# Optimization experiments

Measured on AMD Instinct MI355X. Metric: run time of the kernel, lower is better.

The kernel has to match this reference:

```python
import jax, jax.numpy as jnp
import numpy as np

N, E, G = 50000, 400000, 2048
H, C = 4, 64            # heads, hidden per head
IN, ED, TASKS = 29, 6, 12
HC = H * C


def setup_inputs() -> dict:
    key = jax.random.key(0)
    ks = jax.random.split(key, 20)
    s = 0.1
    f32 = jnp.float32
    inp = {
        'x': jax.random.normal(ks[0], (N, IN), f32),
        'edge_index': jax.random.randint(ks[1], (2, E), 0, N),
        'edge_attr': jax.random.normal(ks[2], (E, ED), f32),
        'batch': jnp.sort(jax.random.randint(ks[3], (N,), 0, G)),
        # layer 1 (in=29 -> H*C=256)
        'W1': jax.random.normal(ks[4], (IN, HC), f32) * s,
        'as1': jax.random.normal(ks[5], (1, H, C), f32) * s,
        'ad1': jax.random.normal(ks[6], (1, H, C), f32) * s,
        'We1': jax.random.normal(ks[7], (ED, HC), f32) * s,
        'ae1': jax.random.normal(ks[8], (1, H, C), f32) * s,
        'b1': jnp.zeros((HC,), f32),
        # layer 2 (in=256 -> 256)
        'W2': jax.random.normal(ks[9], (HC, HC), f32) * s,
        'as2': jax.random.normal(ks[10], (1, H, C), f32) * s,
        'ad2': jax.random.normal(ks[11], (1, H, C), f32) * s,
        'We2': jax.random.normal(ks[12], (ED, HC), f32) * s,
        'ae2': jax.random.normal(ks[13], (1, H, C), f32) * s,
        'b2': jnp.zeros((HC,), f32),
        # readout linear (256 -> 12)
        'Wl': jax.random.normal(ks[14], (HC, TASKS), f32) * s,
        'bl': jnp.zeros((TASKS,), f32),
    }
    return inp


def _gat_conv(x, src, dst, eattr, W, a_src, a_dst, We, a_e, b):
    """PyG GATConv, concat=True, leaky_relu slope 0.2, self-loops already appended."""
    h = (x @ W).reshape(N, H, C)                      # [N,H,C]
    al_s = jnp.sum(h * a_src, axis=-1)                # [N,H]
    al_d = jnp.sum(h * a_dst, axis=-1)                # [N,H]
    he = (eattr @ We).reshape(-1, H, C)               # [Etot,H,C]
    al_e = jnp.sum(he * a_e, axis=-1)                 # [Etot,H]
    alpha = al_s[src] + al_d[dst] + al_e              # [Etot,H]
    alpha = jax.nn.leaky_relu(alpha, negative_slope=0.2)
    # segment softmax over incoming edges of each dst node
    amax = jax.ops.segment_max(alpha, dst, num_segments=N)
    ex = jnp.exp(alpha - amax[dst])
    denom = jax.ops.segment_sum(ex, dst, num_segments=N)
    alpha = ex / (denom[dst] + 1e-16)
    msg = h[src] * alpha[:, :, None]                  # [Etot,H,C]
    out = jax.ops.segment_sum(msg, dst, num_segments=N)
    return out.reshape(N, HC) + b


def reference(x, edge_index, edge_attr, batch,
              W1, as1, ad1, We1, ae1, b1,
              W2, as2, ad2, We2, ae2, b2, Wl, bl):
    # add self-loops with edge_attr fill = mean over existing edges (PyG default)
    loop = jnp.arange(N)
    src = jnp.concatenate([edge_index[0], loop])
    dst = jnp.concatenate([edge_index[1], loop])
    mean_e = jnp.mean(edge_attr, axis=0, keepdims=True)
    eattr = jnp.concatenate([edge_attr, jnp.broadcast_to(mean_e, (N, ED))], axis=0)

    h = _gat_conv(x, src, dst, eattr, W1, as1, ad1, We1, ae1, b1)
    h = jax.nn.relu(h)
    h = _gat_conv(h, src, dst, eattr, W2, as2, ad2, We2, ae2, b2)
    h = jax.nn.relu(h)

    # global mean pool over graphs
    sums = jax.ops.segment_sum(h, batch, num_segments=G)      # [G,HC]
    cnt = jax.ops.segment_sum(jnp.ones((N,), h.dtype), batch, num_segments=G)
    pooled = sums / jnp.maximum(cnt, 1.0)[:, None]
    return pooled @ Wl + bl
```

## Files before the change

kernel.cpp:

```cpp
#include <hip/hip_runtime.h>
#include <math.h>

static constexpr int NN = 50000;
static constexpr int EE = 400000;
static constexpr int GG = 2048;
static constexpr int TASKS = 12;

typedef __attribute__((ext_vector_type(8))) short short8;
typedef __attribute__((ext_vector_type(4))) float floatx4;

__device__ __forceinline__ unsigned short f2bf(float f) {
  unsigned u = __float_as_uint(f);
  u = u + 0x7fffu + ((u >> 16) & 1u);
  return (unsigned short)(u >> 16);
}
__device__ __forceinline__ float bflo(unsigned u) { return __uint_as_float(u << 16); }
__device__ __forceinline__ float bfhi(unsigned u) { return __uint_as_float(u & 0xffff0000u); }

static constexpr int NBDEG = (EE + 255) / 256;
static constexpr int NBMEAN = 256;
static constexpr int NBX = (NN * 4 + 255) / 256;
static constexpr int NW1 = 32;
static constexpr int NW2 = 256;
__global__ void k_pre(const int* __restrict__ dst, const float* __restrict__ ea,
                      const float* __restrict__ x, const float* __restrict__ W1,
                      const float* __restrict__ W2, int* __restrict__ deg,
                      float* __restrict__ msum, unsigned short* __restrict__ xb,
                      unsigned short* __restrict__ w1t, unsigned short* __restrict__ w2t) {
  const int b = blockIdx.x;
  const int t = threadIdx.x;
  if (b < NBDEG) {
    int e = b * 256 + t;
    if (e < EE) atomicAdd(&deg[dst[e]], 1);
  } else if (b < NBDEG + NBMEAN) {
    float s[6] = {0, 0, 0, 0, 0, 0};
    for (int e = (b - NBDEG) * 256 + t; e < EE; e += NBMEAN * 256) {
#pragma unroll
      for (int d = 0; d < 6; d++) s[d] += ea[(size_t)e * 6 + d];
    }
    __shared__ float ls[6];
    if (t < 6) ls[t] = 0.f;
    __syncthreads();
#pragma unroll
    for (int d = 0; d < 6; d++) atomicAdd(&ls[d], s[d]);
    __syncthreads();
    if (t < 6) atomicAdd(&msum[t], ls[t]);
  } else if (b < NBDEG + NBMEAN + NBX) {
    int i = (b - NBDEG - NBMEAN) * 256 + t;
    if (i < NN * 4) {
      int n = i >> 2, seg = i & 3;
      unsigned short v[8];
#pragma unroll
      for (int j = 0; j < 8; j++) {
        int k = seg * 8 + j;
        v[j] = (k < 29) ? f2bf(x[(size_t)n * 29 + k]) : (unsigned short)0;
      }
      *(short8*)(xb + (size_t)n * 32 + seg * 8) = *(short8*)v;
    }
  } else if (b < NBDEG + NBMEAN + NBX + NW1) {
    int i = (b - NBDEG - NBMEAN - NBX) * 256 + t;
    int row = i >> 5, k = i & 31;
    unsigned short v = (k < 29) ? f2bf(W1[(size_t)k * 256 + row]) : (unsigned short)0;
    w1t[((row >> 4) * 4 + (k >> 3)) * 128 + (row & 15) * 8 + (k & 7)] = v;
  } else {
    int i = (b - NBDEG - NBMEAN - NBX - NW1) * 256 + t;
    int row = i >> 8, k = i & 255;
    w2t[((row >> 4) * 32 + (k >> 3)) * 128 + (row & 15) * 8 + (k & 7)] = f2bf(W2[(size_t)k * 256 + row]);
  }
}

__global__ void k_scan1(const int* __restrict__ deg, int* __restrict__ rowptr, int* __restrict__ bsums) {
  __shared__ int sh[256];
  int i = blockIdx.x * 256 + threadIdx.x;
  int v = (i < NN) ? deg[i] : 0;
  sh[threadIdx.x] = v;
  __syncthreads();
  for (int off = 1; off < 256; off <<= 1) {
    int t = (threadIdx.x >= off) ? sh[threadIdx.x - off] : 0;
    __syncthreads();
    sh[threadIdx.x] += t;
    __syncthreads();
  }
  if (i < NN) rowptr[i] = sh[threadIdx.x] - v;
  if (threadIdx.x == 255) bsums[blockIdx.x] = sh[255];
}

__global__ void k_scan23(int* __restrict__ rowptr, const int* __restrict__ bsums, int nb) {
  __shared__ int sh[256];
  const int t = threadIdx.x;
  sh[t] = (t < nb) ? bsums[t] : 0;
  __syncthreads();
  for (int off = 1; off < 256; off <<= 1) {
    int tv = (t >= off) ? sh[t - off] : 0;
    __syncthreads();
    sh[t] += tv;
    __syncthreads();
  }
  const int add = (blockIdx.x == 0) ? 0 : sh[blockIdx.x - 1];
  int i = blockIdx.x * 256 + t;
  if (i < NN) rowptr[i] += add;
  if (i == 0) rowptr[NN] = EE;
}

template <int KP>
__device__ __forceinline__ void gemm_body(
    int bx, const unsigned short* __restrict__ A, const unsigned short* __restrict__ Bt,
    const float* __restrict__ a_s, const float* __restrict__ a_d,
    unsigned short* __restrict__ Y, float* __restrict__ als, float* __restrict__ ald, int M) {
  __shared__ __align__(16) unsigned short Ash[64 * KP];
  const int tid = threadIdx.x;
  const int lane = tid & 63;
  const int w = tid >> 6;
  const int l15 = lane & 15;
  const int quad = lane >> 4;
  const int row0 = bx * 64;

  constexpr int STEPS = (64 * KP * 2) / (256 * 16);
  {
    const char* Ab = (const char*)(A + (size_t)row0 * KP);
    uint4 stg[STEPS];
#pragma unroll
    for (int s = 0; s < STEPS; s++) stg[s] = *(const uint4*)(Ab + s * 4096 + tid * 16);
#pragma unroll
    for (int s = 0; s < STEPS; s++) {
      int o = s * 4096 + tid * 16;
      int row = o / (KP * 2);
      *(uint4*)((char*)Ash + (o ^ ((row & 7) << 4))) = stg[s];
    }
  }

  floatx4 acc[4][4];
#pragma unroll
  for (int i = 0; i < 4; i++)
#pragma unroll
    for (int j = 0; j < 4; j++) acc[i][j] = {0.f, 0.f, 0.f, 0.f};

  const unsigned short* pb[4];
#pragma unroll
  for (int j = 0; j < 4; j++)
    pb[j] = Bt + (size_t)((w * 4 + j) * (KP / 8) + quad) * 128 + l15 * 8;

  constexpr int NPH = KP / 32;
  short8 bfr[2][4];
#pragma unroll
  for (int j = 0; j < 4; j++) bfr[0][j] = *(const short8*)pb[j];

  __syncthreads();

#pragma unroll
  for (int ph = 0; ph < NPH; ph++) {
    const int cur = ph & 1, nxt = cur ^ 1;
    if (ph + 1 < NPH) {
#pragma unroll
      for (int j = 0; j < 4; j++) {
        pb[j] += 512;
        bfr[nxt][j] = *(const short8*)pb[j];
      }
    }
    short8 af[4];
#pragma unroll
    for (int i = 0; i < 4; i++) {
      int lin = (i * 16 + l15) * (KP * 2) + ph * 64 + quad * 16;
      af[i] = *(const short8*)((const char*)Ash + (lin ^ (((lin / (KP * 2)) & 7) << 4)));
    }
#pragma unroll
    for (int i = 0; i < 4; i++)
#pragma unroll
      for (int j = 0; j < 4; j++)
        acc[i][j] = __builtin_amdgcn_mfma_f32_16x16x32_bf16(af[i], bfr[cur][j], acc[i][j], 0, 0, 0);
  }
  float asc[4], adc[4];
#pragma unroll
  for (int j = 0; j < 4; j++) {
    asc[j] = a_s[w * 64 + j * 16 + l15];
    adc[j] = a_d[w * 64 + j * 16 + l15];
  }
#pragma unroll
  for (int i = 0; i < 4; i++) {
#pragma unroll
    for (int r = 0; r < 4; r++) {
      const int row = row0 + i * 16 + quad * 4 + r;
      unsigned ub[4];
      float hv[4];
#pragma unroll
      for (int j = 0; j < 4; j++) {
        ub[j] = f2bf(acc[i][j][r]);
        hv[j] = __uint_as_float(ub[j] << 16);
      }
      if (row < M) {
#pragma unroll
        for (int j = 0; j < 4; j++) Y[(size_t)row * 256 + w * 64 + j * 16 + l15] = (unsigned short)ub[j];
      }
      float ps = hv[0] * asc[0] + hv[1] * asc[1] + hv[2] * asc[2] + hv[3] * asc[3];
      float pd = hv[0] * adc[0] + hv[1] * adc[1] + hv[2] * adc[2] + hv[3] * adc[3];
#pragma unroll
      for (int off = 1; off < 16; off <<= 1) {
        ps += __shfl_xor(ps, off, 64);
        pd += __shfl_xor(pd, off, 64);
      }
      if (l15 == 0 && row < M) {
        als[row * 4 + w] = ps;
        ald[row * 4 + w] = pd;
      }
    }
  }
}

static constexpr int GB = (NN + 63) / 64;

__global__ __launch_bounds__(256, 2) void k_scatgemm1(
    const int* __restrict__ ei, const int* __restrict__ rowptr, int* __restrict__ cursor,
    int* __restrict__ csrc, int* __restrict__ eslot, const float* __restrict__ We1,
    const float* __restrict__ ae1, const float* __restrict__ We2, const float* __restrict__ ae2,
    const float* __restrict__ msum, float* __restrict__ p1, float* __restrict__ p2,
    const unsigned short* __restrict__ xb, const unsigned short* __restrict__ w1t,
    const float* __restrict__ as1, const float* __restrict__ ad1,
    unsigned short* __restrict__ hb, float* __restrict__ als, float* __restrict__ ald) {
  const int b = blockIdx.x;
  const int t = threadIdx.x;
  if (b < NBDEG) {
    int e = b * 256 + t;
    if (e >= EE) return;
    int s = ei[e];
    int d = ei[EE + e];
    int p = atomicAdd(&cursor[d], 1);
    int slot = rowptr[d] + p;
    csrc[slot] = s;
    eslot[e] = slot;
  } else if (b < NBDEG + 2) {
    const int layer = b - NBDEG;
    const float* We = layer ? We2 : We1;
    const float* ae = layer ? ae2 : ae1;
    float* params = layer ? p2 : p1;
    __shared__ float vsh[24];
    if (t < 24) {
      int d = t >> 2, h = t & 3;
      float s = 0.f;
      for (int c = 0; c < 64; c++) s += We[d * 256 + h * 64 + c] * ae[h * 64 + c];
      vsh[t] = s;
      params[t] = s;
    }
    __syncthreads();
    if (t < 4) {
      float s = 0.f;
      const float invE = 1.0f / (float)EE;
#pragma unroll
      for (int d = 0; d < 6; d++) s += (msum[d] * invE) * vsh[d * 4 + t];
      params[24 + t] = s;
    }
  } else {
    gemm_body<32>(b - NBDEG - 2, xb, w1t, as1, ad1, hb, als, ald, NN);
  }
}

__global__ __launch_bounds__(256, 2) void k_gemm2(
    const unsigned short* __restrict__ A, const unsigned short* __restrict__ Bt,
    const float* __restrict__ a_s, const float* __restrict__ a_d,
    unsigned short* __restrict__ Y, float* __restrict__ als, float* __restrict__ ald) {
  gemm_body<256>(blockIdx.x, A, Bt, a_s, a_d, Y, als, ald, NN);
}

__device__ __forceinline__ float leaky02(float x) { return x > 0.f ? x : 0.2f * x; }

__global__ void k_edge(const int* __restrict__ ei, const float* __restrict__ ea,
                       const float* __restrict__ als, const float* __restrict__ ald,
                       const int* __restrict__ eslot, const float* __restrict__ params,
                       float* __restrict__ exa) {
  int e = blockIdx.x * blockDim.x + threadIdx.x;
  if (e >= EE) return;
  int src = ei[e], dst = ei[EE + e];
  float4 s4 = *(const float4*)(als + (size_t)src * 4);
  float4 d4 = *(const float4*)(ald + (size_t)dst * 4);
  float ed[6];
#pragma unroll
  for (int d = 0; d < 6; d++) ed[d] = ea[(size_t)e * 6 + d];
  float sl[4] = {s4.x + d4.x, s4.y + d4.y, s4.z + d4.z, s4.w + d4.w};
  float out[4];
#pragma unroll
  for (int h = 0; h < 4; h++) {
    float x = sl[h];
#pragma unroll
    for (int d = 0; d < 6; d++) x += ed[d] * params[d * 4 + h];
    out[h] = __expf(leaky02(x));
  }
  *(float4*)(exa + (size_t)eslot[e] * 4) = make_float4(out[0], out[1], out[2], out[3]);
}

__global__ __launch_bounds__(256) void k_agg(
    const unsigned short* __restrict__ hinb, const float* __restrict__ als,
    const float* __restrict__ ald, const int* __restrict__ rowptr, const int* __restrict__ csrc,
    const float* __restrict__ exa, const float* __restrict__ params, const float* __restrict__ bias,
    unsigned short* __restrict__ houtb) {
  const int lane = threadIdx.x & 63;
  const int n = blockIdx.x * 4 + (threadIdx.x >> 6);
  if (n >= NN) return;
  const int half = lane >> 5;
  const int sl = lane & 31;
  const int head = sl >> 3;

  float acc[8];
  float ssum;
  {
    float slg = leaky02(als[n * 4 + head] + ald[n * 4 + head] + params[24 + head]);
    float exs = __expf(slg);
    float wgt = (half == 0) ? exs : 0.f;
    ssum = wgt;
    uint4 uv = *(const uint4*)(hinb + (size_t)n * 256 + sl * 8);
    acc[0] = bflo(uv.x) * wgt;
    acc[1] = bfhi(uv.x) * wgt;
    acc[2] = bflo(uv.y) * wgt;
    acc[3] = bfhi(uv.y) * wgt;
    acc[4] = bflo(uv.z) * wgt;
    acc[5] = bfhi(uv.z) * wgt;
    acc[6] = bflo(uv.w) * wgt;
    acc[7] = bfhi(uv.w) * wgt;
  }
  const int end = rowptr[n + 1];
  int s = rowptr[n] + half;
  while (s < end) {
    int sid[4];
    float ex[4];
#pragma unroll
    for (int k = 0; k < 4; k++) {
      const int q = s + 2 * k;
      const bool v = q < end;
      const int idx = v ? q : end - 1;
      sid[k] = csrc[idx];
      ex[k] = v ? exa[(size_t)idx * 4 + head] : 0.f;
    }
    uint4 r[4];
#pragma unroll
    for (int k = 0; k < 4; k++) {
      r[k] = make_uint4(0u, 0u, 0u, 0u);
      if (s + 2 * k < end) r[k] = *(const uint4*)(hinb + (size_t)sid[k] * 256 + sl * 8);
    }
#pragma unroll
    for (int k = 0; k < 4; k++) {
      acc[0] += bflo(r[k].x) * ex[k];
      acc[1] += bfhi(r[k].x) * ex[k];
      acc[2] += bflo(r[k].y) * ex[k];
      acc[3] += bfhi(r[k].y) * ex[k];
      acc[4] += bflo(r[k].z) * ex[k];
      acc[5] += bfhi(r[k].z) * ex[k];
      acc[6] += bflo(r[k].w) * ex[k];
      acc[7] += bfhi(r[k].w) * ex[k];
      ssum += ex[k];
    }
    s += 8;
  }
#pragma unroll
  for (int j = 0; j < 8; j++) acc[j] += __shfl_xor(acc[j], 32, 64);
  ssum += __shfl_xor(ssum, 32, 64);
  if (half == 0) {
    const float inv = 1.f / (ssum + 1e-16f);
    float4 b0 = *(const float4*)(bias + sl * 8);
    float4 b1 = *(const float4*)(bias + sl * 8 + 4);
    const float bb[8] = {b0.x, b0.y, b0.z, b0.w, b1.x, b1.y, b1.z, b1.w};
    uint p[4];
#pragma unroll
    for (int j = 0; j < 4; j++) {
      float e0 = fmaxf(acc[2 * j] * inv + bb[2 * j], 0.f);
      float e1 = fmaxf(acc[2 * j + 1] * inv + bb[2 * j + 1], 0.f);
      p[j] = (uint)f2bf(e0) | ((uint)f2bf(e1) << 16);
    }
    *(uint4*)(houtb + (size_t)n * 256 + sl * 8) = make_uint4(p[0], p[1], p[2], p[3]);
  }
}

__global__ __launch_bounds__(256) void k_pool(const unsigned short* __restrict__ hb,
                                              const int* __restrict__ batch,
                                              const float* __restrict__ Wl,
                                              const float* __restrict__ bl,
                                              float* __restrict__ out) {
  int g = blockIdx.x;
  int t = threadIdx.x;
  int lo = 0, hi = NN;
  while (lo < hi) {
    int mid = (lo + hi) >> 1;
    if (batch[mid] < g) lo = mid + 1; else hi = mid;
  }
  int start = lo;
  hi = NN;
  while (lo < hi) {
    int mid = (lo + hi) >> 1;
    if (batch[mid] < g + 1) lo = mid + 1; else hi = mid;
  }
  int end = lo;
  const int mid2 = start + ((end - start) >> 1);
  __shared__ float sp[256], sq[256];
  {
    const int c = t & 127;
    const int hseg = t >> 7;
    const int a = hseg ? mid2 : start;
    const int b = hseg ? end : mid2;
    float s0 = 0.f, s1 = 0.f;
    for (int n2 = a; n2 < b; n2++) {
      uint u = ((const uint*)(hb + (size_t)n2 * 256))[c];
      s0 += bflo(u);
      s1 += bfhi(u);
    }
    float* dst = hseg ? sq : sp;
    dst[2 * c] = s0;
    dst[2 * c + 1] = s1;
  }
  __syncthreads();
  if (t < TASKS) {
    float invc = 1.f / fmaxf((float)(end - start), 1.f);
    float o = bl[t];
    for (int c = 0; c < 256; c++) o += (sp[c] + sq[c]) * invc * Wl[c * 12 + t];
    out[(size_t)g * 12 + t] = o;
  }
}

extern "C" void kernel_launch(void* const* d_in, const int* in_sizes, int n_in,
                              void* d_out, int out_size, void* d_ws, size_t ws_size,
                              hipStream_t stream) {
  const float* x = (const float*)d_in[0];
  const int* ei = (const int*)d_in[1];
  const float* ea = (const float*)d_in[2];
  const int* batch = (const int*)d_in[3];
  const float* W1 = (const float*)d_in[4];
  const float* as1 = (const float*)d_in[5];
  const float* ad1 = (const float*)d_in[6];
  const float* We1 = (const float*)d_in[7];
  const float* ae1 = (const float*)d_in[8];
  const float* b1 = (const float*)d_in[9];
  const float* W2 = (const float*)d_in[10];
  const float* as2 = (const float*)d_in[11];
  const float* ad2 = (const float*)d_in[12];
  const float* We2 = (const float*)d_in[13];
  const float* ae2 = (const float*)d_in[14];
  const float* b2 = (const float*)d_in[15];
  const float* Wl = (const float*)d_in[16];
  const float* bl = (const float*)d_in[17];
  float* out = (float*)d_out;

  char* ws = (char*)d_ws;
  size_t off = 0;
  auto take = [&](size_t bytes) -> char* {
    char* p = ws + off;
    off = (off + bytes + 255) & ~(size_t)255;
    return p;
  };
  float* msum = (float*)take(8 * 4);
  int* deg = (int*)take((size_t)NN * 4);
  int* cursor = (int*)take((size_t)NN * 4);
  size_t zero_end = off;
  int* rowptr = (int*)take((size_t)(NN + 1) * 4);
  int* bsums = (int*)take(256 * 4);
  int* csrc = (int*)take((size_t)EE * 4);
  int* eslot = (int*)take((size_t)EE * 4);
  float* exa = (float*)take((size_t)EE * 4 * 4);
  float* p1 = (float*)take(32 * 4);
  float* p2 = (float*)take(32 * 4);
  float* als = (float*)take((size_t)NN * 4 * 4);
  float* ald = (float*)take((size_t)NN * 4 * 4);
  unsigned short* hb = (unsigned short*)take((size_t)NN * 256 * 2);
  unsigned short* ab = (unsigned short*)take((size_t)NN * 256 * 2);
  unsigned short* xb = (unsigned short*)take((size_t)NN * 32 * 2);
  unsigned short* w1t = (unsigned short*)take((size_t)256 * 32 * 2);
  unsigned short* w2t = (unsigned short*)take((size_t)256 * 256 * 2);
  (void)ws_size;

  hipMemsetAsync(ws, 0, zero_end, stream);

  const int nbN = (NN + 255) / 256;
  const int nbE = (EE + 255) / 256;

  k_pre<<<NBDEG + NBMEAN + NBX + NW1 + NW2, 256, 0, stream>>>(ei + EE, ea, x, W1, W2,
                                                              deg, msum, xb, w1t, w2t);
  k_scan1<<<nbN, 256, 0, stream>>>(deg, rowptr, bsums);
  k_scan23<<<nbN, 256, 0, stream>>>(rowptr, bsums, nbN);

  k_scatgemm1<<<NBDEG + 2 + GB, 256, 0, stream>>>(ei, rowptr, cursor, csrc, eslot,
                                                  We1, ae1, We2, ae2, msum, p1, p2,
                                                  xb, w1t, as1, ad1, hb, als, ald);

  k_edge<<<nbE, 256, 0, stream>>>(ei, ea, als, ald, eslot, p1, exa);
  k_agg<<<NN / 4, 256, 0, stream>>>(hb, als, ald, rowptr, csrc, exa, p1, b1, ab);

  k_gemm2<<<GB, 256, 0, stream>>>(ab, w2t, as2, ad2, hb, als, ald);
  k_edge<<<nbE, 256, 0, stream>>>(ei, ea, als, ald, eslot, p2, exa);
  k_agg<<<NN / 4, 256, 0, stream>>>(hb, als, ald, rowptr, csrc, exa, p2, b2, ab);

  k_pool<<<GG, 256, 0, stream>>>(ab, batch, Wl, bl, out);
}
```

Before: 300.2 us.

## Fuse edge-logit kernel into aggregation and precompute CSR-ordered edge terms

Removes both k_edge launches. The per-edge attribute contribution for both layers is now computed once during the CSR scatter and stored in slot order. k_agg gathers als for each source itself and computes the exp of the attention logits inline. The edge-param computation moves into the scan kernel so p1/p2 are ready before the scatter. The GEMM also gets a deeper B-fragment prefetch (triple buffer) and double-buffered A-fragment LDS loads. The cost is an extra scattered als gather and the exp work inside the aggregation loop, in exchange for dropping two full edge passes and the exa/eslot traffic.

```diff
diff --git a/kernel.cpp b/kernel.cpp
--- a/kernel.cpp
+++ b/kernel.cpp
@@ -69,20 +69,50 @@
   }
 }
 
-__global__ void k_scan1(const int* __restrict__ deg, int* __restrict__ rowptr, int* __restrict__ bsums) {
+static constexpr int NBS = (NN + 255) / 256;
+
+__global__ void k_scan1(const int* __restrict__ deg, int* __restrict__ rowptr,
+                        int* __restrict__ bsums, const float* __restrict__ We1,
+                        const float* __restrict__ ae1, const float* __restrict__ We2,
+                        const float* __restrict__ ae2, const float* __restrict__ msum,
+                        float* __restrict__ p1, float* __restrict__ p2) {
+  const int t = threadIdx.x;
+  if (blockIdx.x >= NBS) {
+    const int layer = blockIdx.x - NBS;
+    const float* We = layer ? We2 : We1;
+    const float* ae = layer ? ae2 : ae1;
+    float* params = layer ? p2 : p1;
+    __shared__ float vsh[24];
+    if (t < 24) {
+      int d = t >> 2, h = t & 3;
+      float s = 0.f;
+      for (int c = 0; c < 64; c++) s += We[d * 256 + h * 64 + c] * ae[h * 64 + c];
+      vsh[t] = s;
+      params[t] = s;
+    }
+    __syncthreads();
+    if (t < 4) {
+      float s = 0.f;
+      const float invE = 1.0f / (float)EE;
+#pragma unroll
+      for (int d = 0; d < 6; d++) s += (msum[d] * invE) * vsh[d * 4 + t];
+      params[24 + t] = s;
+    }
+    return;
+  }
   __shared__ int sh[256];
-  int i = blockIdx.x * 256 + threadIdx.x;
+  int i = blockIdx.x * 256 + t;
   int v = (i < NN) ? deg[i] : 0;
-  sh[threadIdx.x] = v;
+  sh[t] = v;
   __syncthreads();
   for (int off = 1; off < 256; off <<= 1) {
-    int t = (threadIdx.x >= off) ? sh[threadIdx.x - off] : 0;
-    __syncthreads();
-    sh[threadIdx.x] += t;
-    __syncthreads();
-  }
-  if (i < NN) rowptr[i] = sh[threadIdx.x] - v;
-  if (threadIdx.x == 255) bsums[blockIdx.x] = sh[255];
+    int tv = (t >= off) ? sh[t - off] : 0;
+    __syncthreads();
+    sh[t] += tv;
+    __syncthreads();
+  }
+  if (i < NN) rowptr[i] = sh[t] - v;
+  if (t == 255) bsums[blockIdx.x] = sh[255];
 }
 
 __global__ void k_scan23(int* __restrict__ rowptr, const int* __restrict__ bsums, int nb) {
@@ -141,33 +171,44 @@
     pb[j] = Bt + (size_t)((w * 4 + j) * (KP / 8) + quad) * 128 + l15 * 8;
 
   constexpr int NPH = KP / 32;
-  short8 bfr[2][4];
+  short8 bfr[3][4];
 #pragma unroll
   for (int j = 0; j < 4; j++) bfr[0][j] = *(const short8*)pb[j];
+  if (NPH > 1) {
+#pragma unroll
+    for (int j = 0; j < 4; j++) {
+      pb[j] += 512;
+      bfr[1][j] = *(const short8*)pb[j];
+    }
+  }
 
   __syncthreads();
 
+  auto ldA = [&](int ph, short8 (&dst)[4]) {
+#pragma unroll
+    for (int i = 0; i < 4; i++) {
+      int lin = (i * 16 + l15) * (KP * 2) + ph * 64 + quad * 16;
+      dst[i] = *(const short8*)((const char*)Ash + (lin ^ ((l15 & 7) << 4)));
+    }
+  };
+  short8 af[2][4];
+  ldA(0, af[0]);
+
 #pragma unroll
   for (int ph = 0; ph < NPH; ph++) {
-    const int cur = ph & 1, nxt = cur ^ 1;
-    if (ph + 1 < NPH) {
+    if (ph + 2 < NPH) {
 #pragma unroll
       for (int j = 0; j < 4; j++) {
         pb[j] += 512;
-        bfr[nxt][j] = *(const short8*)pb[j];
-      }
-    }
-    short8 af[4];
-#pragma unroll
-    for (int i = 0; i < 4; i++) {
-      int lin = (i * 16 + l15) * (KP * 2) + ph * 64 + quad * 16;
-      af[i] = *(const short8*)((const char*)Ash + (lin ^ (((lin / (KP * 2)) & 7) << 4)));
-    }
+        bfr[(ph + 2) % 3][j] = *(const short8*)pb[j];
+      }
+    }
+    if (ph + 1 < NPH) ldA(ph + 1, af[(ph + 1) & 1]);
 #pragma unroll
     for (int i = 0; i < 4; i++)
 #pragma unroll
       for (int j = 0; j < 4; j++)
-        acc[i][j] = __builtin_amdgcn_mfma_f32_16x16x32_bf16(af[i], bfr[cur][j], acc[i][j], 0, 0, 0);
+        acc[i][j] = __builtin_amdgcn_mfma_f32_16x16x32_bf16(af[ph & 1][i], bfr[ph % 3][j], acc[i][j], 0, 0, 0);
   }
   float asc[4], adc[4];
 #pragma unroll
@@ -210,9 +251,9 @@
 
 __global__ __launch_bounds__(256, 2) void k_scatgemm1(
     const int* __restrict__ ei, const int* __restrict__ rowptr, int* __restrict__ cursor,
-    int* __restrict__ csrc, int* __restrict__ eslot, const float* __restrict__ We1,
-    const float* __restrict__ ae1, const float* __restrict__ We2, const float* __restrict__ ae2,
-    const float* __restrict__ msum, float* __restrict__ p1, float* __restrict__ p2,
+    int* __restrict__ csrc, const float* __restrict__ ea,
+    const float* __restrict__ p1, const float* __restrict__ p2,
+    float* __restrict__ ed1, float* __restrict__ ed2,
     const unsigned short* __restrict__ xb, const unsigned short* __restrict__ w1t,
     const float* __restrict__ as1, const float* __restrict__ ad1,
     unsigned short* __restrict__ hb, float* __restrict__ als, float* __restrict__ ald) {
@@ -226,30 +267,22 @@
     int p = atomicAdd(&cursor[d], 1);
     int slot = rowptr[d] + p;
     csrc[slot] = s;
-    eslot[e] = slot;
-  } else if (b < NBDEG + 2) {
-    const int layer = b - NBDEG;
-    const float* We = layer ? We2 : We1;
-    const float* ae = layer ? ae2 : ae1;
-    float* params = layer ? p2 : p1;
-    __shared__ float vsh[24];
-    if (t < 24) {
-      int d = t >> 2, h = t & 3;
-      float s = 0.f;
-      for (int c = 0; c < 64; c++) s += We[d * 256 + h * 64 + c] * ae[h * 64 + c];
-      vsh[t] = s;
-      params[t] = s;
-    }
-    __syncthreads();
-    if (t < 4) {
-      float s = 0.f;
-      const float invE = 1.0f / (float)EE;
-#pragma unroll
-      for (int d = 0; d < 6; d++) s += (msum[d] * invE) * vsh[d * 4 + t];
-      params[24 + t] = s;
-    }
+    float ed6[6];
+#pragma unroll
+    for (int d6 = 0; d6 < 6; d6++) ed6[d6] = ea[(size_t)e * 6 + d6];
+    float c1[4] = {0.f, 0.f, 0.f, 0.f}, c2[4] = {0.f, 0.f, 0.f, 0.f};
+#pragma unroll
+    for (int h = 0; h < 4; h++) {
+#pragma unroll
+      for (int d6 = 0; d6 < 6; d6++) {
+        c1[h] += ed6[d6] * p1[d6 * 4 + h];
+        c2[h] += ed6[d6] * p2[d6 * 4 + h];
+      }
+    }
+    *(float4*)(ed1 + (size_t)slot * 4) = make_float4(c1[0], c1[1], c1[2], c1[3]);
+    *(float4*)(ed2 + (size_t)slot * 4) = make_float4(c2[0], c2[1], c2[2], c2[3]);
   } else {
-    gemm_body<32>(b - NBDEG - 2, xb, w1t, as1, ad1, hb, als, ald, NN);
+    gemm_body<32>(b - NBDEG, xb, w1t, as1, ad1, hb, als, ald, NN);
   }
 }
 
@@ -262,34 +295,10 @@
 
 __device__ __forceinline__ float leaky02(float x) { return x > 0.f ? x : 0.2f * x; }
 
-__global__ void k_edge(const int* __restrict__ ei, const float* __restrict__ ea,
-                       const float* __restrict__ als, const float* __restrict__ ald,
-                       const int* __restrict__ eslot, const float* __restrict__ params,
-                       float* __restrict__ exa) {
-  int e = blockIdx.x * blockDim.x + threadIdx.x;
-  if (e >= EE) return;
-  int src = ei[e], dst = ei[EE + e];
-  float4 s4 = *(const float4*)(als + (size_t)src * 4);
-  float4 d4 = *(const float4*)(ald + (size_t)dst * 4);
-  float ed[6];
-#pragma unroll
-  for (int d = 0; d < 6; d++) ed[d] = ea[(size_t)e * 6 + d];
-  float sl[4] = {s4.x + d4.x, s4.y + d4.y, s4.z + d4.z, s4.w + d4.w};
-  float out[4];
-#pragma unroll
-  for (int h = 0; h < 4; h++) {
-    float x = sl[h];
-#pragma unroll
-    for (int d = 0; d < 6; d++) x += ed[d] * params[d * 4 + h];
-    out[h] = __expf(leaky02(x));
-  }
-  *(float4*)(exa + (size_t)eslot[e] * 4) = make_float4(out[0], out[1], out[2], out[3]);
-}
-
 __global__ __launch_bounds__(256) void k_agg(
     const unsigned short* __restrict__ hinb, const float* __restrict__ als,
     const float* __restrict__ ald, const int* __restrict__ rowptr, const int* __restrict__ csrc,
-    const float* __restrict__ exa, const float* __restrict__ params, const float* __restrict__ bias,
+    const float* __restrict__ edc, const float* __restrict__ params, const float* __restrict__ bias,
     unsigned short* __restrict__ houtb) {
   const int lane = threadIdx.x & 63;
   const int n = blockIdx.x * 4 + (threadIdx.x >> 6);
@@ -298,10 +307,11 @@
   const int sl = lane & 31;
   const int head = sl >> 3;
 
+  const float aldn = ald[n * 4 + head];
   float acc[8];
   float ssum;
   {
-    float slg = leaky02(als[n * 4 + head] + ald[n * 4 + head] + params[24 + head]);
+    float slg = leaky02(als[n * 4 + head] + aldn + params[24 + head]);
     float exs = __expf(slg);
     float wgt = (half == 0) ? exs : 0.f;
     ssum = wgt;
@@ -319,15 +329,18 @@
   int s = rowptr[n] + half;
   while (s < end) {
     int sid[4];
-    float ex[4];
+    float edv[4];
 #pragma unroll
     for (int k = 0; k < 4; k++) {
       const int q = s + 2 * k;
       const bool v = q < end;
       const int idx = v ? q : end - 1;
       sid[k] = csrc[idx];
-      ex[k] = v ? exa[(size_t)idx * 4 + head] : 0.f;
-    }
+      edv[k] = v ? edc[(size_t)idx * 4 + head] : 0.f;
+    }
+    float alv[4];
+#pragma unroll
+    for (int k = 0; k < 4; k++) alv[k] = als[(size_t)sid[k] * 4 + head];
     uint4 r[4];
 #pragma unroll
     for (int k = 0; k < 4; k++) {
@@ -336,15 +349,16 @@
     }
 #pragma unroll
     for (int k = 0; k < 4; k++) {
-      acc[0] += bflo(r[k].x) * ex[k];
-      acc[1] += bfhi(r[k].x) * ex[k];
-      acc[2] += bflo(r[k].y) * ex[k];
-      acc[3] += bfhi(r[k].y) * ex[k];
-      acc[4] += bflo(r[k].z) * ex[k];
-      acc[5] += bfhi(r[k].z) * ex[k];
-      acc[6] += bflo(r[k].w) * ex[k];
-      acc[7] += bfhi(r[k].w) * ex[k];
-      ssum += ex[k];
+      const float ex = (s + 2 * k < end) ? __expf(leaky02(alv[k] + aldn + edv[k])) : 0.f;
+      acc[0] += bflo(r[k].x) * ex;
+      acc[1] += bfhi(r[k].x) * ex;
+      acc[2] += bflo(r[k].y) * ex;
+      acc[3] += bfhi(r[k].y) * ex;
+      acc[4] += bflo(r[k].z) * ex;
+      acc[5] += bfhi(r[k].z) * ex;
+      acc[6] += bflo(r[k].w) * ex;
+      acc[7] += bfhi(r[k].w) * ex;
+      ssum += ex;
     }
     s += 8;
   }
@@ -449,8 +463,8 @@
   int* rowptr = (int*)take((size_t)(NN + 1) * 4);
   int* bsums = (int*)take(256 * 4);
   int* csrc = (int*)take((size_t)EE * 4);
-  int* eslot = (int*)take((size_t)EE * 4);
-  float* exa = (float*)take((size_t)EE * 4 * 4);
+  float* ed1 = (float*)take((size_t)EE * 4 * 4);
+  float* ed2 = (float*)take((size_t)EE * 4 * 4);
   float* p1 = (float*)take(32 * 4);
   float* p2 = (float*)take(32 * 4);
   float* als = (float*)take((size_t)NN * 4 * 4);
@@ -464,24 +478,18 @@
 
   hipMemsetAsync(ws, 0, zero_end, stream);
 
-  const int nbN = (NN + 255) / 256;
-  const int nbE = (EE + 255) / 256;
-
   k_pre<<<NBDEG + NBMEAN + NBX + NW1 + NW2, 256, 0, stream>>>(ei + EE, ea, x, W1, W2,
                                                               deg, msum, xb, w1t, w2t);
-  k_scan1<<<nbN, 256, 0, stream>>>(deg, rowptr, bsums);
-  k_scan23<<<nbN, 256, 0, stream>>>(rowptr, bsums, nbN);
-
-  k_scatgemm1<<<NBDEG + 2 + GB, 256, 0, stream>>>(ei, rowptr, cursor, csrc, eslot,
-                                                  We1, ae1, We2, ae2, msum, p1, p2,
-                                                  xb, w1t, as1, ad1, hb, als, ald);
-
-  k_edge<<<nbE, 256, 0, stream>>>(ei, ea, als, ald, eslot, p1, exa);
-  k_agg<<<NN / 4, 256, 0, stream>>>(hb, als, ald, rowptr, csrc, exa, p1, b1, ab);
+  k_scan1<<<NBS + 2, 256, 0, stream>>>(deg, rowptr, bsums, We1, ae1, We2, ae2, msum, p1, p2);
+  k_scan23<<<NBS, 256, 0, stream>>>(rowptr, bsums, NBS);
+
+  k_scatgemm1<<<NBDEG + GB, 256, 0, stream>>>(ei, rowptr, cursor, csrc, ea, p1, p2,
+                                              ed1, ed2, xb, w1t, as1, ad1, hb, als, ald);
+
+  k_agg<<<NN / 4, 256, 0, stream>>>(hb, als, ald, rowptr, csrc, ed1, p1, b1, ab);
 
   k_gemm2<<<GB, 256, 0, stream>>>(ab, w2t, as2, ad2, hb, als, ald);
-  k_edge<<<nbE, 256, 0, stream>>>(ei, ea, als, ald, eslot, p2, exa);
-  k_agg<<<NN / 4, 256, 0, stream>>>(hb, als, ald, rowptr, csrc, exa, p2, b2, ab);
+  k_agg<<<NN / 4, 256, 0, stream>>>(hb, als, ald, rowptr, csrc, ed2, p2, b2, ab);
 
   k_pool<<<GG, 256, 0, stream>>>(ab, batch, Wl, bl, out);
 }
```

After: 286.8 us. 1.05x faster.
